# Kernel optimization log

Hardware: AMD Instinct MI355X
Metric: run time of the kernel (lower is better)

The kernel has to match this reference:

```python
import jax, jax.numpy as jnp
import numpy as np
from jax.ops import segment_sum, segment_max

N = 20000   # nodes per node type (glom, imm)
E = 320000  # edges per edge type (avg degree 16)
D = 256     # feature dim (in == out, required by GIN's (1+eps)*x + aggr)
LN_EPS = 1e-5


def _ln_relu(x, gamma, beta):
    mu = jnp.mean(x, axis=-1, keepdims=True)
    var = jnp.mean((x - mu) ** 2, axis=-1, keepdims=True)
    return jax.nn.relu((x - mu) * jax.lax.rsqrt(var + LN_EPS) * gamma + beta)


def _forward(x_glom, x_imm, ew_gg, ea_ig, W_gcn, b_gcn, Wl, bl, Wr, br, att, We,
             b_gat, eps, W_gin, b_gin, gamma, beta, ei_gg, ei_ig, ei_gi):
    # ---- GCNConv on (glom->glom): add_self_loops=True, edge_weight=ew_gg ----
    src, dst = ei_gg[0], ei_gg[1]
    xw = x_glom @ W_gcn                                   # [N, D]
    deg = segment_sum(ew_gg, dst, num_segments=N) + 1.0   # +1 for self-loop weight
    dinv = jax.lax.rsqrt(deg)                             # [N]
    coef = dinv[src] * ew_gg * dinv[dst]                  # [E] symmetric gcn_norm
    out_gcn = segment_sum(coef[:, None] * xw[src], dst, num_segments=N)
    out_gcn = out_gcn + (dinv * dinv)[:, None] * xw + b_gcn  # self-loop + bias

    # ---- GATv2Conv on (imm->glom): heads=1, edge_dim=1, no self loops ----
    s, d = ei_ig[0], ei_ig[1]
    hl = x_imm @ Wl + bl          # lin_l on source  [N, D]
    hr = x_glom @ Wr + br         # lin_r on target  [N, D]
    he = ea_ig @ We               # lin_edge         [E, D]
    z = jax.nn.leaky_relu(hl[s] + hr[d] + he, 0.2)
    logits = z @ att              # [E]
    m = segment_max(logits, d, num_segments=N)            # stable segment softmax
    ex = jnp.exp(logits - m[d])
    denom = segment_sum(ex, d, num_segments=N)
    alpha = ex / denom[d]
    out_gat = segment_sum(alpha[:, None] * hl[s], d, num_segments=N) + b_gat

    # ---- GINConv on (glom->imm): nn = Linear, train_eps ----
    s2, d2 = ei_gi[0], ei_gi[1]
    agg = segment_sum(x_glom[s2], d2, num_segments=N)     # sum aggregation
    out_gin = ((1.0 + eps[0]) * x_imm + agg) @ W_gin + b_gin

    # HeteroConv(aggr='sum') across edge types per destination node type,
    # then shared LayerNorm + ReLU
    glom = _ln_relu(out_gcn + out_gat, gamma, beta)
    imm = _ln_relu(out_gin, gamma, beta)
    return glom, imm


def setup_inputs() -> dict:
    key = jax.random.key(0)
    k = jax.random.split(key, 13)
    s = 0.06  # ~ glorot-ish scale for D=256
    return {
        'x_glom': jax.random.normal(k[0], (N, D), jnp.float32),
        'x_imm': jax.random.normal(k[1], (N, D), jnp.float32),
        'ew_gg': jax.random.uniform(k[2], (E,), jnp.float32),
        'ea_ig': jax.random.normal(k[3], (E, 1), jnp.float32),
        'W_gcn': jax.random.normal(k[4], (D, D), jnp.float32) * s,
        'b_gcn': jnp.zeros((D,), jnp.float32),
        'Wl': jax.random.normal(k[5], (D, D), jnp.float32) * s,
        'bl': jnp.zeros((D,), jnp.float32),
        'Wr': jax.random.normal(k[6], (D, D), jnp.float32) * s,
        'br': jnp.zeros((D,), jnp.float32),
        'att': jax.random.normal(k[7], (D,), jnp.float32) * s,
        'We': jax.random.normal(k[8], (1, D), jnp.float32) * s,
        'b_gat': jnp.zeros((D,), jnp.float32),
        'eps': jnp.zeros((1,), jnp.float32),
        'W_gin': jax.random.normal(k[9], (D, D), jnp.float32) * s,
        'b_gin': jnp.zeros((D,), jnp.float32),
        'gamma': jnp.ones((D,), jnp.float32),
        'beta': jnp.zeros((D,), jnp.float32),
        'ei_gg': jax.random.randint(k[10], (2, E), 0, N),
        'ei_ig': jax.random.randint(k[11], (2, E), 0, N),
        'ei_gi': jax.random.randint(k[12], (2, E), 0, N),
    }


def reference(x_glom, x_imm, ew_gg, ea_ig, W_gcn, b_gcn, Wl, bl, Wr, br, att, We,
              b_gat, eps, W_gin, b_gin, gamma, beta, ei_gg, ei_ig, ei_gi):
    return _forward(x_glom, x_imm, ew_gg, ea_ig, W_gcn, b_gcn, Wl, bl, Wr, br,
                    att, We, b_gat, eps, W_gin, b_gin, gamma, beta,
                    ei_gg, ei_ig, ei_gi)
```

## Files before the change

kernel.cpp:

```cpp
#include <hip/hip_runtime.h>


constexpr int D = 256;

typedef __attribute__((ext_vector_type(4))) float f32x4v;
typedef __attribute__((ext_vector_type(8))) short short8;

__device__ __forceinline__ float4 ld4(const float* p) {
    return *reinterpret_cast<const float4*>(p);
}
__device__ __forceinline__ void st4(float* p, float4 v) {
    *reinterpret_cast<float4*>(p) = v;
}
__device__ __forceinline__ unsigned short f2bf(float f) {
    unsigned u = __float_as_uint(f);
    u = u + 0x7FFFu + ((u >> 16) & 1u);
    return (unsigned short)(u >> 16);
}
__device__ __forceinline__ float bf2f(unsigned short u) {
    return __uint_as_float(((unsigned)u) << 16);
}
__device__ __forceinline__ float4 ldb4(const unsigned short* p) {
    ushort4 u = *reinterpret_cast<const ushort4*>(p);
    return make_float4(bf2f(u.x), bf2f(u.y), bf2f(u.z), bf2f(u.w));
}
__device__ __forceinline__ float wave_sum(float p) {
#pragma unroll
    for (int off = 32; off > 0; off >>= 1) p += __shfl_xor(p, off, 64);
    return p;
}
__device__ __forceinline__ float gat_partial(float4 h, float4 hrv, float ea,
                                             float4 We4, float4 att4) {
    float z, pp = 0.f;
    z = h.x + hrv.x + ea * We4.x; z *= (z > 0.f) ? 1.0f : 0.2f; pp += z * att4.x;
    z = h.y + hrv.y + ea * We4.y; z *= (z > 0.f) ? 1.0f : 0.2f; pp += z * att4.y;
    z = h.z + hrv.z + ea * We4.z; z *= (z > 0.f) ? 1.0f : 0.2f; pp += z * att4.z;
    z = h.w + hrv.w + ea * We4.w; z *= (z > 0.f) ? 1.0f : 0.2f; pp += z * att4.w;
    return pp;
}

__global__ __launch_bounds__(256)
void k_front(const float* __restrict__ x_glom, const float* __restrict__ x_imm,
             unsigned short* __restrict__ xb_glom, unsigned short* __restrict__ xb_imm,
             const float* __restrict__ W0, const float* __restrict__ W1,
             const float* __restrict__ W2, const float* __restrict__ W3,
             unsigned short* __restrict__ Wt,
             const int* __restrict__ ei_gg, const int* __restrict__ ei_ig,
             const int* __restrict__ ei_gi, const float* __restrict__ ew_gg,
             int* __restrict__ counts, int* __restrict__ rank,
             float* __restrict__ degsum,
             int n4, int nbCast, int nbHist, int E, int N)
{
    int bx = blockIdx.x;
    if (bx < 2 * nbCast) {
        bool second = (bx >= nbCast);
        int i = (second ? bx - nbCast : bx) * 256 + threadIdx.x;
        if (i < n4) {
            const float* x = second ? x_imm : x_glom;
            unsigned short* y = second ? xb_imm : xb_glom;
            float4 v = ld4(x + (size_t)i * 4);
            ushort4 o;
            o.x = f2bf(v.x); o.y = f2bf(v.y); o.z = f2bf(v.z); o.w = f2bf(v.w);
            *reinterpret_cast<ushort4*>(y + (size_t)i * 4) = o;
        }
        return;
    }
    bx -= 2 * nbCast;
    if (bx < 1024) {
        int w = bx >> 8;
        int i = ((bx & 255) << 8) + threadIdx.x;
        const float* W = (w == 0) ? W0 : (w == 1) ? W1 : (w == 2) ? W2 : W3;
        int c = i >> 8, k = i & 255;
        Wt[(size_t)w * D * D + i] = f2bf(W[k * D + c]);
        return;
    }
    bx -= 1024;
    {
        int t = bx / nbHist;
        int e = (bx - t * nbHist) * 256 + threadIdx.x;
        if (e >= E) return;
        const int* ei = (t == 0) ? ei_gg : (t == 1) ? ei_ig : ei_gi;
        int d = ei[E + e];
        rank[(size_t)t * E + e] = atomicAdd(&counts[t * N + d], 1);
        if (t == 0) atomicAdd(&degsum[d], ew_gg[e]);
    }
}

__global__ __launch_bounds__(256)
void k_scan_tile(const int* __restrict__ counts, int* __restrict__ rows,
                 int* __restrict__ partials, int N, int TPT)
{
    int t = blockIdx.y, tile = blockIdx.x;
    int i = tile * 256 + threadIdx.x;
    __shared__ int sh[256];
    int v = (i < N) ? counts[(size_t)t * N + i] : 0;
    sh[threadIdx.x] = v;
    __syncthreads();
#pragma unroll
    for (int off = 1; off < 256; off <<= 1) {
        int add = (threadIdx.x >= off) ? sh[threadIdx.x - off] : 0;
        __syncthreads();
        sh[threadIdx.x] += add;
        __syncthreads();
    }
    if (i < N) rows[(size_t)t * (N + 1) + i] = sh[threadIdx.x] - v;
    if (threadIdx.x == 255) partials[t * TPT + tile] = sh[255];
}

__global__ __launch_bounds__(128)
void k_scan_part(int* __restrict__ partials, int TPT)
{
    int t = blockIdx.x;
    __shared__ int sh[128];
    int v = (threadIdx.x < TPT) ? partials[t * TPT + threadIdx.x] : 0;
    sh[threadIdx.x] = v;
    __syncthreads();
#pragma unroll
    for (int off = 1; off < 128; off <<= 1) {
        int add = (threadIdx.x >= off) ? sh[threadIdx.x - off] : 0;
        __syncthreads();
        sh[threadIdx.x] += add;
        __syncthreads();
    }
    if (threadIdx.x < TPT) partials[t * TPT + threadIdx.x] = sh[threadIdx.x] - v;
}

__global__ void k_scan_final(int* __restrict__ rows, const int* __restrict__ partials,
                             int N, int TPT, int E)
{
    int i = blockIdx.x * 256 + threadIdx.x;
    if (i >= 3 * N) return;
    int t = i / N, j = i - t * N;
    rows[(size_t)t * (N + 1) + j] += partials[t * TPT + (j >> 8)];
    if (j == 0) rows[(size_t)t * (N + 1) + N] = E;
}

__global__ __launch_bounds__(256)
void k_mid(
           const unsigned short* __restrict__ xbg,
           const unsigned short* __restrict__ xbi,
           const unsigned short* __restrict__ Wt,
           const float* __restrict__ degsum,
           const float* __restrict__ br, const float* __restrict__ bl,
           unsigned short* __restrict__ xws, unsigned short* __restrict__ hr,
           unsigned short* __restrict__ hl,
           const int* __restrict__ ei_gg, const int* __restrict__ ei_ig,
           const int* __restrict__ ei_gi, const float* __restrict__ ew_gg,
           const float* __restrict__ ea_ig,
           const int* __restrict__ rows, const int* __restrict__ rank,
           int2* __restrict__ pk_gcn, int2* __restrict__ pk_gat,
           int* __restrict__ src_gin,
           int nbProjRow, int nbProj, int nbE, int E, int N, int M)
{
    int bx = blockIdx.x;
    if (bx < nbProj) {
        int brow = bx / 12;
        int yy   = bx - brow * 12;
        const int lane = threadIdx.x & 63;
        const int wave = threadIdx.x >> 6;
        const int lr = lane & 15;
        const int lk = lane >> 4;
        const int row0 = brow * 256 + wave * 64;

        const unsigned short* A;
        const unsigned short* Bt0;
        int col0;
        if (yy < 8) { A = xbg; Bt0 = Wt;             col0 = yy * 64; }
        else        { A = xbi; Bt0 = Wt + 2 * D * D; col0 = (yy - 8) * 64; }

        const unsigned short* ap[4];
#pragma unroll
        for (int rf = 0; rf < 4; ++rf) {
            int arow = row0 + rf * 16 + lr;
            int arow_c = (arow < M) ? arow : (M - 1);
            ap[rf] = A + (size_t)arow_c * D + lk * 8;
        }
        const unsigned short* bp = Bt0 + (size_t)(col0 + lr) * D + lk * 8;

        f32x4v acc[4][4] = {};
#pragma unroll
        for (int k0 = 0; k0 < 256; k0 += 32) {
            short8 af[4], bf[4];
#pragma unroll
            for (int rf = 0; rf < 4; ++rf)
                af[rf] = *reinterpret_cast<const short8*>(ap[rf] + k0);
#pragma unroll
            for (int nf = 0; nf < 4; ++nf)
                bf[nf] = *reinterpret_cast<const short8*>(bp + (size_t)nf * 16 * D + k0);
#pragma unroll
            for (int rf = 0; rf < 4; ++rf)
#pragma unroll
                for (int nf = 0; nf < 4; ++nf)
                    acc[rf][nf] = __builtin_amdgcn_mfma_f32_16x16x32_bf16(
                        af[rf], bf[nf], acc[rf][nf], 0, 0, 0);
        }

#pragma unroll
        for (int nf = 0; nf < 4; ++nf) {
            int c = col0 + nf * 16 + lr;
            unsigned short* dst;
            int cc;
            float bv;
            bool scaled;
            if (yy < 8) {
                if (c < 256) { dst = xws; cc = c;       bv = 0.f;    scaled = true;  }
                else         { dst = hr;  cc = c - 256; bv = br[cc]; scaled = false; }
            } else           { dst = hl;  cc = c;       bv = bl[cc]; scaled = false; }
#pragma unroll
            for (int rf = 0; rf < 4; ++rf) {
#pragma unroll
                for (int i = 0; i < 4; ++i) {
                    int r = row0 + rf * 16 + 4 * lk + i;
                    if (r < M) {
                        float sc = scaled ? rsqrtf(1.0f + degsum[r]) : 1.0f;
                        dst[(size_t)r * D + cc] = f2bf(acc[rf][nf][i] * sc + bv);
                    }
                }
            }
        }
        return;
    }
    int sx = bx - nbProj;
    int t = sx / nbE;
    int e = (sx - t * nbE) * 256 + threadIdx.x;
    if (e >= E) return;
    if (t == 0) {
        int s = ei_gg[e], d = ei_gg[E + e];
        int pos = rows[d] + rank[e];
        pk_gcn[pos] = make_int2(s, __float_as_int(ew_gg[e]));
    } else if (t == 1) {
        int s = ei_ig[e], d = ei_ig[E + e];
        int pos = rows[(N + 1) + d] + rank[(size_t)E + e];
        pk_gat[pos] = make_int2(s, __float_as_int(ea_ig[e]));
    } else {
        int s = ei_gi[e], d = ei_gi[E + e];
        int pos = rows[2 * (N + 1) + d] + rank[2 * (size_t)E + e];
        src_gin[pos] = s;
    }
}

__global__ __launch_bounds__(256)
void k_gin_gemm_ln(const unsigned short* __restrict__ A,
                   const unsigned short* __restrict__ Bt,
                   const float* __restrict__ bias,
                   const float* __restrict__ gamma, const float* __restrict__ beta,
                   float* __restrict__ out, int M)
{
    __shared__ float lds_s[4][64];
    __shared__ float lds_q[4][64];
    const int lane = threadIdx.x & 63;
    const int wave = threadIdx.x >> 6;
    const int lr = lane & 15;
    const int lk = lane >> 4;
    const int row0 = blockIdx.x * 64;
    const int col0 = wave * 64;

    const unsigned short* ap[4];
#pragma unroll
    for (int rf = 0; rf < 4; ++rf) {
        int arow = row0 + rf * 16 + lr;
        int arow_c = (arow < M) ? arow : (M - 1);
        ap[rf] = A + (size_t)arow_c * D + lk * 8;
    }
    const unsigned short* bp = Bt + (size_t)(col0 + lr) * D + lk * 8;

    f32x4v acc[4][4] = {};
#pragma unroll
    for (int k0 = 0; k0 < 256; k0 += 32) {
        short8 af[4], bf[4];
#pragma unroll
        for (int rf = 0; rf < 4; ++rf)
            af[rf] = *reinterpret_cast<const short8*>(ap[rf] + k0);
#pragma unroll
        for (int nf = 0; nf < 4; ++nf)
            bf[nf] = *reinterpret_cast<const short8*>(bp + (size_t)nf * 16 * D + k0);
#pragma unroll
        for (int rf = 0; rf < 4; ++rf)
#pragma unroll
            for (int nf = 0; nf < 4; ++nf)
                acc[rf][nf] = __builtin_amdgcn_mfma_f32_16x16x32_bf16(
                    af[rf], bf[nf], acc[rf][nf], 0, 0, 0);
    }

    float bv[4], gv[4], be[4];
#pragma unroll
    for (int nf = 0; nf < 4; ++nf) {
        int c = col0 + nf * 16 + lr;
        bv[nf] = bias[c]; gv[nf] = gamma[c]; be[nf] = beta[c];
    }

#pragma unroll
    for (int rf = 0; rf < 4; ++rf) {
        float ps[4], pq[4];
#pragma unroll
        for (int i = 0; i < 4; ++i) {
            float s = 0.f, q = 0.f;
#pragma unroll
            for (int nf = 0; nf < 4; ++nf) {
                float v = acc[rf][nf][i] + bv[nf];
                acc[rf][nf][i] = v;
                s += v; q += v * v;
            }
            ps[i] = s; pq[i] = q;
        }
#pragma unroll
        for (int off = 1; off < 16; off <<= 1) {
#pragma unroll
            for (int i = 0; i < 4; ++i) {
                ps[i] += __shfl_xor(ps[i], off, 64);
                pq[i] += __shfl_xor(pq[i], off, 64);
            }
        }
        if (lr == 0) {
#pragma unroll
            for (int i = 0; i < 4; ++i) {
                lds_s[wave][rf * 16 + lk * 4 + i] = ps[i];
                lds_q[wave][rf * 16 + lk * 4 + i] = pq[i];
            }
        }
    }
    __syncthreads();

#pragma unroll
    for (int rf = 0; rf < 4; ++rf) {
#pragma unroll
        for (int i = 0; i < 4; ++i) {
            int rl = rf * 16 + 4 * lk + i;
            float s = lds_s[0][rl] + lds_s[1][rl] + lds_s[2][rl] + lds_s[3][rl];
            float q = lds_q[0][rl] + lds_q[1][rl] + lds_q[2][rl] + lds_q[3][rl];
            float mu  = s * (1.0f / 256.0f);
            float var = q * (1.0f / 256.0f) - mu * mu;
            float rs  = rsqrtf(var + 1e-5f);
            int r = row0 + rl;
            if (r < M) {
#pragma unroll
                for (int nf = 0; nf < 4; ++nf) {
                    out[(size_t)r * D + col0 + nf * 16 + lr] =
                        fmaxf(0.f, (acc[rf][nf][i] - mu) * rs * gv[nf] + be[nf]);
                }
            }
        }
    }
}

__global__ __launch_bounds__(256)
void k_gather_fused(const unsigned short* __restrict__ xws,
                    const unsigned short* __restrict__ hl,
                    const unsigned short* __restrict__ hr,
                    const float* __restrict__ degsum,
                    const int* __restrict__ rows_gcn, const int2* __restrict__ pk_gcn,
                    const int* __restrict__ rows_gat, const int2* __restrict__ pk_gat,
                    const float* __restrict__ We, const float* __restrict__ att,
                    const float* __restrict__ b_gcn, const float* __restrict__ b_gat,
                    const float* __restrict__ gamma, const float* __restrict__ beta,
                    float* __restrict__ glom_out,
                    const unsigned short* __restrict__ xb_glom,
                    const float* __restrict__ x_imm, const float* __restrict__ eps,
                    const int* __restrict__ rows_gin, const int* __restrict__ src_gin,
                    unsigned short* __restrict__ agg,
                    int N)
{
    int gw   = __builtin_amdgcn_readfirstlane((blockIdx.x * 256 + threadIdx.x) >> 6);
    int lane = threadIdx.x & 63;

    if (gw < N) {
        int node = gw;
        float4 We4  = ld4(&We[lane * 4]);
        float4 att4 = ld4(&att[lane * 4]);
        float4 hrv  = ldb4(&hr[(size_t)node * D + lane * 4]);

        float di = rsqrtf(1.0f + degsum[node]);
        float4 acc = ldb4(&xws[(size_t)node * D + lane * 4]);
        float4 g0  = ld4(&b_gcn[lane * 4]);
        float4 a0  = ld4(&b_gat[lane * 4]);
        acc.x = di * acc.x + g0.x + a0.x;
        acc.y = di * acc.y + g0.y + a0.y;
        acc.z = di * acc.z + g0.z + a0.z;
        acc.w = di * acc.w + g0.w + a0.w;

        int p  = rows_gcn[node];
        int p1 = rows_gcn[node + 1];
        int2 pkn[4];
        if (p + 4 <= p1) {
#pragma unroll
            for (int j = 0; j < 4; ++j) pkn[j] = pk_gcn[p + j];
        }
        while (p + 4 <= p1) {
            int2 pkc[4];
#pragma unroll
            for (int j = 0; j < 4; ++j) pkc[j] = pkn[j];
            p += 4;
            if (p + 4 <= p1) {
#pragma unroll
                for (int j = 0; j < 4; ++j) pkn[j] = pk_gcn[p + j];
            }
            float cf[4];
            float4 v[4];
#pragma unroll
            for (int j = 0; j < 4; ++j) cf[j] = __int_as_float(pkc[j].y) * di;
#pragma unroll
            for (int j = 0; j < 4; ++j) v[j] = ldb4(&xws[(size_t)pkc[j].x * D + lane * 4]);
#pragma unroll
            for (int j = 0; j < 4; ++j) {
                acc.x += cf[j] * v[j].x; acc.y += cf[j] * v[j].y;
                acc.z += cf[j] * v[j].z; acc.w += cf[j] * v[j].w;
            }
        }
        for (; p < p1; ++p) {
            int2 pk = pk_gcn[p];
            float cx = __int_as_float(pk.y) * di;
            float4 v = ldb4(&xws[(size_t)pk.x * D + lane * 4]);
            acc.x += cx * v.x; acc.y += cx * v.y;
            acc.z += cx * v.z; acc.w += cx * v.w;
        }

        int q  = rows_gat[node];
        int q1 = rows_gat[node + 1];
        int has = (q1 > q);
        float m = -3.4e38f, den = 0.f;
        float4 ag = make_float4(0.f, 0.f, 0.f, 0.f);
        int2 qkn[4];
        if (q + 4 <= q1) {
#pragma unroll
            for (int j = 0; j < 4; ++j) qkn[j] = pk_gat[q + j];
        }
        while (q + 4 <= q1) {
            int2 qkc[4];
#pragma unroll
            for (int j = 0; j < 4; ++j) qkc[j] = qkn[j];
            q += 4;
            if (q + 4 <= q1) {
#pragma unroll
                for (int j = 0; j < 4; ++j) qkn[j] = pk_gat[q + j];
            }
            float4 h[4];
            float pp[4];
#pragma unroll
            for (int j = 0; j < 4; ++j) h[j] = ldb4(&hl[(size_t)qkc[j].x * D + lane * 4]);
#pragma unroll
            for (int j = 0; j < 4; ++j)
                pp[j] = wave_sum(gat_partial(h[j], hrv, __int_as_float(qkc[j].y), We4, att4));
            float mb = fmaxf(fmaxf(pp[0], pp[1]), fmaxf(pp[2], pp[3]));
            float mn = fmaxf(m, mb);
            float scale = __expf(m - mn);
            float x[4];
#pragma unroll
            for (int j = 0; j < 4; ++j) x[j] = __expf(pp[j] - mn);
            den = den * scale + (x[0] + x[1]) + (x[2] + x[3]);
            float axx = 0.f, ayy = 0.f, azz = 0.f, aww = 0.f;
#pragma unroll
            for (int j = 0; j < 4; ++j) {
                axx += x[j] * h[j].x; ayy += x[j] * h[j].y;
                azz += x[j] * h[j].z; aww += x[j] * h[j].w;
            }
            ag.x = ag.x * scale + axx; ag.y = ag.y * scale + ayy;
            ag.z = ag.z * scale + azz; ag.w = ag.w * scale + aww;
            m = mn;
        }
        for (; q < q1; ++q) {
            int2 pk = pk_gat[q];
            float4 h = ldb4(&hl[(size_t)pk.x * D + lane * 4]);
            float pp = wave_sum(gat_partial(h, hrv, __int_as_float(pk.y), We4, att4));
            float mn = fmaxf(m, pp);
            float scale = __expf(m - mn);
            float ex = __expf(pp - mn);
            den = den * scale + ex;
            ag.x = ag.x * scale + ex * h.x;
            ag.y = ag.y * scale + ex * h.y;
            ag.z = ag.z * scale + ex * h.z;
            ag.w = ag.w * scale + ex * h.w;
            m = mn;
        }
        if (has) {
            float inv = 1.0f / den;
            acc.x += ag.x * inv; acc.y += ag.y * inv;
            acc.z += ag.z * inv; acc.w += ag.w * inv;
        }

        float s_ = acc.x + acc.y + acc.z + acc.w;
        float sq = acc.x * acc.x + acc.y * acc.y + acc.z * acc.z + acc.w * acc.w;
#pragma unroll
        for (int off = 32; off > 0; off >>= 1) {
            s_ += __shfl_xor(s_, off, 64);
            sq += __shfl_xor(sq, off, 64);
        }
        float mu  = s_ * (1.0f / 256.0f);
        float var = sq * (1.0f / 256.0f) - mu * mu;
        float rs  = rsqrtf(var + 1e-5f);
        float4 g = ld4(&gamma[lane * 4]);
        float4 b = ld4(&beta[lane * 4]);
        float4 o;
        o.x = fmaxf(0.f, (acc.x - mu) * rs * g.x + b.x);
        o.y = fmaxf(0.f, (acc.y - mu) * rs * g.y + b.y);
        o.z = fmaxf(0.f, (acc.z - mu) * rs * g.z + b.z);
        o.w = fmaxf(0.f, (acc.w - mu) * rs * g.w + b.w);
        st4(&glom_out[(size_t)node * D + lane * 4], o);
    } else if (gw < 2 * N) {
        int node = gw - N;
        float c = 1.0f + eps[0];
        float4 acc = ld4(&x_imm[(size_t)node * D + lane * 4]);
        acc.x *= c; acc.y *= c; acc.z *= c; acc.w *= c;
        int p  = rows_gin[node];
        int p1 = rows_gin[node + 1];
        int sn[4];
        if (p + 4 <= p1) {
#pragma unroll
            for (int j = 0; j < 4; ++j) sn[j] = src_gin[p + j];
        }
        while (p + 4 <= p1) {
            int sc[4];
#pragma unroll
            for (int j = 0; j < 4; ++j) sc[j] = sn[j];
            p += 4;
            if (p + 4 <= p1) {
#pragma unroll
                for (int j = 0; j < 4; ++j) sn[j] = src_gin[p + j];
            }
            float4 v[4];
#pragma unroll
            for (int j = 0; j < 4; ++j) v[j] = ldb4(&xb_glom[(size_t)sc[j] * D + lane * 4]);
            acc.x += (v[0].x + v[1].x) + (v[2].x + v[3].x);
            acc.y += (v[0].y + v[1].y) + (v[2].y + v[3].y);
            acc.z += (v[0].z + v[1].z) + (v[2].z + v[3].z);
            acc.w += (v[0].w + v[1].w) + (v[2].w + v[3].w);
        }
        for (; p < p1; ++p) {
            int sx = src_gin[p];
            float4 v = ldb4(&xb_glom[(size_t)sx * D + lane * 4]);
            acc.x += v.x; acc.y += v.y; acc.z += v.z; acc.w += v.w;
        }
        ushort4 o;
        o.x = f2bf(acc.x); o.y = f2bf(acc.y); o.z = f2bf(acc.z); o.w = f2bf(acc.w);
        *reinterpret_cast<ushort4*>(agg + (size_t)node * D + lane * 4) = o;
    }
}

extern "C" void kernel_launch(void* const* d_in, const int* in_sizes, int n_in,
                              void* d_out, int out_size, void* d_ws, size_t ws_size,
                              hipStream_t stream)
{
    const float* x_glom = (const float*)d_in[0];
    const float* x_imm  = (const float*)d_in[1];
    const float* ew_gg  = (const float*)d_in[2];
    const float* ea_ig  = (const float*)d_in[3];
    const float* W_gcn  = (const float*)d_in[4];
    const float* b_gcn  = (const float*)d_in[5];
    const float* Wl     = (const float*)d_in[6];
    const float* bl     = (const float*)d_in[7];
    const float* Wr     = (const float*)d_in[8];
    const float* br     = (const float*)d_in[9];
    const float* att    = (const float*)d_in[10];
    const float* We     = (const float*)d_in[11];
    const float* b_gat  = (const float*)d_in[12];
    const float* eps    = (const float*)d_in[13];
    const float* W_gin  = (const float*)d_in[14];
    const float* b_gin  = (const float*)d_in[15];
    const float* gamma  = (const float*)d_in[16];
    const float* beta   = (const float*)d_in[17];
    const int*   ei_gg  = (const int*)d_in[18];
    const int*   ei_ig  = (const int*)d_in[19];
    const int*   ei_gi  = (const int*)d_in[20];

    const int N = in_sizes[0] / D;
    const int E = in_sizes[2];
    const size_t ND = (size_t)N * D;
    const int TPT = (N + 255) / 256;

    char* base = (char*)d_ws;
    size_t off = 0;
    auto alloc = [&](size_t bytes) {
        void* p = base + off;
        off = (off + bytes + 255) & ~(size_t)255;
        return p;
    };
    unsigned short* xb_glom = (unsigned short*)alloc(ND * 2);
    unsigned short* xb_imm  = (unsigned short*)alloc(ND * 2);
    unsigned short* xws_b   = (unsigned short*)alloc(ND * 2);
    unsigned short* hl_b    = (unsigned short*)alloc(ND * 2);
    unsigned short* hr_b    = (unsigned short*)alloc(ND * 2);
    unsigned short* agg_b   = (unsigned short*)alloc(ND * 2);
    unsigned short* Wt      = (unsigned short*)alloc(4 * D * D * 2);
    int*   counts  = (int*)alloc(3 * (size_t)N * 4 + (size_t)N * 4);
    float* degsum  = (float*)(counts + 3 * (size_t)N);
    int*   rows    = (int*)alloc(3 * (size_t)(N + 1) * 4);
    int*   parts   = (int*)alloc(3 * (size_t)TPT * 4);
    int*   rank    = (int*)alloc(3 * (size_t)E * 4);
    int2*  pk_gcn  = (int2*)alloc((size_t)E * 8);
    int2*  pk_gat  = (int2*)alloc((size_t)E * 8);
    int*   src_gin = (int*)alloc((size_t)E * 4);

    float* glom_out = (float*)d_out;
    float* imm_out  = (float*)d_out + ND;

    const int n4      = (int)(ND / 4);
    const int nbCast  = (n4 + 255) / 256;
    const int nbHist  = (E + 255) / 256;
    const int nb_3n   = (3 * N + 255) / 256;
    const int nb_2nw  = (2 * N + 3) / 4;
    const int nbProjRow = (N + 255) / 256;
    const int nbProj    = nbProjRow * 12;

    hipMemsetAsync(counts, 0, 4 * (size_t)N * 4, stream);
    k_front<<<2 * nbCast + 1024 + 3 * nbHist, 256, 0, stream>>>(
        x_glom, x_imm, xb_glom, xb_imm,
        W_gcn, Wr, Wl, W_gin, Wt,
        ei_gg, ei_ig, ei_gi, ew_gg,
        counts, rank, degsum, n4, nbCast, nbHist, E, N);
    k_scan_tile<<<dim3(TPT, 3), 256, 0, stream>>>(counts, rows, parts, N, TPT);
    k_scan_part<<<3, 128, 0, stream>>>(parts, TPT);
    k_scan_final<<<nb_3n, 256, 0, stream>>>(rows, parts, N, TPT, E);
    k_mid<<<nbProj + 3 * nbHist, 256, 0, stream>>>(
        xb_glom, xb_imm, Wt, degsum, br, bl, xws_b, hr_b, hl_b,
        ei_gg, ei_ig, ei_gi, ew_gg, ea_ig,
        rows, rank, pk_gcn, pk_gat, src_gin,
        nbProjRow, nbProj, nbHist, E, N, N);
    k_gather_fused<<<nb_2nw, 256, 0, stream>>>(
        xws_b, hl_b, hr_b, degsum,
        rows, pk_gcn,
        rows + (N + 1), pk_gat,
        We, att, b_gcn, b_gat, gamma, beta, glom_out,
        xb_glom, x_imm, eps,
        rows + 2 * (N + 1), src_gin, agg_b, N);
    k_gin_gemm_ln<<<(N + 63) / 64, 256, 0, stream>>>(
        agg_b, Wt + 3 * D * D, b_gin, gamma, beta, imm_out, N);
}
```

Before: 240.4 us.

## Apply GIN linear before aggregation and fuse GIN into the gather kernel

Uses linearity to compute x_glom@W_gin and x_imm@W_gin inside the projection GEMM, so the GIN branch becomes a gather-sum of pre-projected rows followed by LayerNorm in the gather kernel. This removes the separate GIN GEMM+LN kernel and the agg intermediate buffer. The gather kernel is also restructured so each wave processes two edges at once, each half-wave loading 8 bf16 values (16 bytes) per lane, with cross-half reductions for the GCN sums and for the GAT online softmax. The histogram blocks are moved to the front of k_front. In exchange the projection GEMM grows from 12 to 20 column tiles per row block, and rounding to bf16 now happens before aggregation rather than after.

```diff
diff --git a/kernel.cpp b/kernel.cpp
--- a/kernel.cpp
+++ b/kernel.cpp
@@ -8,9 +8,6 @@
 
 __device__ __forceinline__ float4 ld4(const float* p) {
     return *reinterpret_cast<const float4*>(p);
-}
-__device__ __forceinline__ void st4(float* p, float4 v) {
-    *reinterpret_cast<float4*>(p) = v;
 }
 __device__ __forceinline__ unsigned short f2bf(float f) {
     unsigned u = __float_as_uint(f);
@@ -20,23 +17,10 @@
 __device__ __forceinline__ float bf2f(unsigned short u) {
     return __uint_as_float(((unsigned)u) << 16);
 }
-__device__ __forceinline__ float4 ldb4(const unsigned short* p) {
-    ushort4 u = *reinterpret_cast<const ushort4*>(p);
-    return make_float4(bf2f(u.x), bf2f(u.y), bf2f(u.z), bf2f(u.w));
-}
-__device__ __forceinline__ float wave_sum(float p) {
-#pragma unroll
-    for (int off = 32; off > 0; off >>= 1) p += __shfl_xor(p, off, 64);
-    return p;
-}
-__device__ __forceinline__ float gat_partial(float4 h, float4 hrv, float ea,
-                                             float4 We4, float4 att4) {
-    float z, pp = 0.f;
-    z = h.x + hrv.x + ea * We4.x; z *= (z > 0.f) ? 1.0f : 0.2f; pp += z * att4.x;
-    z = h.y + hrv.y + ea * We4.y; z *= (z > 0.f) ? 1.0f : 0.2f; pp += z * att4.y;
-    z = h.z + hrv.z + ea * We4.z; z *= (z > 0.f) ? 1.0f : 0.2f; pp += z * att4.z;
-    z = h.w + hrv.w + ea * We4.w; z *= (z > 0.f) ? 1.0f : 0.2f; pp += z * att4.w;
-    return pp;
+__device__ __forceinline__ void ldbf8(const unsigned short* p, float* o) {
+    short8 u = *reinterpret_cast<const short8*>(p);
+#pragma unroll
+    for (int j = 0; j < 8; ++j) o[j] = bf2f((unsigned short)u[j]);
 }
 
 __global__ __launch_bounds__(256)
@@ -52,6 +36,17 @@
              int n4, int nbCast, int nbHist, int E, int N)
 {
     int bx = blockIdx.x;
+    if (bx < 3 * nbHist) {
+        int t = bx / nbHist;
+        int e = (bx - t * nbHist) * 256 + threadIdx.x;
+        if (e >= E) return;
+        const int* ei = (t == 0) ? ei_gg : (t == 1) ? ei_ig : ei_gi;
+        int d = ei[E + e];
+        rank[(size_t)t * E + e] = atomicAdd(&counts[t * N + d], 1);
+        if (t == 0) atomicAdd(&degsum[d], ew_gg[e]);
+        return;
+    }
+    bx -= 3 * nbHist;
     if (bx < 2 * nbCast) {
         bool second = (bx >= nbCast);
         int i = (second ? bx - nbCast : bx) * 256 + threadIdx.x;
@@ -66,23 +61,12 @@
         return;
     }
     bx -= 2 * nbCast;
-    if (bx < 1024) {
+    {
         int w = bx >> 8;
         int i = ((bx & 255) << 8) + threadIdx.x;
         const float* W = (w == 0) ? W0 : (w == 1) ? W1 : (w == 2) ? W2 : W3;
         int c = i >> 8, k = i & 255;
         Wt[(size_t)w * D * D + i] = f2bf(W[k * D + c]);
-        return;
-    }
-    bx -= 1024;
-    {
-        int t = bx / nbHist;
-        int e = (bx - t * nbHist) * 256 + threadIdx.x;
-        if (e >= E) return;
-        const int* ei = (t == 0) ? ei_gg : (t == 1) ? ei_ig : ei_gi;
-        int d = ei[E + e];
-        rank[(size_t)t * E + e] = atomicAdd(&counts[t * N + d], 1);
-        if (t == 0) atomicAdd(&degsum[d], ew_gg[e]);
     }
 }
 
@@ -136,26 +120,26 @@
 }
 
 __global__ __launch_bounds__(256)
-void k_mid(
-           const unsigned short* __restrict__ xbg,
+void k_mid(const unsigned short* __restrict__ xbg,
            const unsigned short* __restrict__ xbi,
            const unsigned short* __restrict__ Wt,
            const float* __restrict__ degsum,
            const float* __restrict__ br, const float* __restrict__ bl,
            unsigned short* __restrict__ xws, unsigned short* __restrict__ hr,
            unsigned short* __restrict__ hl,
+           unsigned short* __restrict__ xgw, unsigned short* __restrict__ xiw,
            const int* __restrict__ ei_gg, const int* __restrict__ ei_ig,
            const int* __restrict__ ei_gi, const float* __restrict__ ew_gg,
            const float* __restrict__ ea_ig,
            const int* __restrict__ rows, const int* __restrict__ rank,
            int2* __restrict__ pk_gcn, int2* __restrict__ pk_gat,
            int* __restrict__ src_gin,
-           int nbProjRow, int nbProj, int nbE, int E, int N, int M)
+           int nbProj, int nbE, int E, int N, int M)
 {
     int bx = blockIdx.x;
     if (bx < nbProj) {
-        int brow = bx / 12;
-        int yy   = bx - brow * 12;
+        int brow = bx / 20;
+        int yy   = bx - brow * 20;
         const int lane = threadIdx.x & 63;
         const int wave = threadIdx.x >> 6;
         const int lr = lane & 15;
@@ -165,8 +149,10 @@
         const unsigned short* A;
         const unsigned short* Bt0;
         int col0;
-        if (yy < 8) { A = xbg; Bt0 = Wt;             col0 = yy * 64; }
-        else        { A = xbi; Bt0 = Wt + 2 * D * D; col0 = (yy - 8) * 64; }
+        if (yy < 8)       { A = xbg; Bt0 = Wt;             col0 = yy * 64; }
+        else if (yy < 12) { A = xbg; Bt0 = Wt + 3 * D * D; col0 = (yy - 8) * 64; }
+        else if (yy < 16) { A = xbi; Bt0 = Wt + 2 * D * D; col0 = (yy - 12) * 64; }
+        else              { A = xbi; Bt0 = Wt + 3 * D * D; col0 = (yy - 16) * 64; }
 
         const unsigned short* ap[4];
 #pragma unroll
@@ -205,7 +191,9 @@
             if (yy < 8) {
                 if (c < 256) { dst = xws; cc = c;       bv = 0.f;    scaled = true;  }
                 else         { dst = hr;  cc = c - 256; bv = br[cc]; scaled = false; }
-            } else           { dst = hl;  cc = c;       bv = bl[cc]; scaled = false; }
+            } else if (yy < 12) { dst = xgw; cc = c;    bv = 0.f;    scaled = false; }
+            else if (yy < 16)   { dst = hl;  cc = c;    bv = bl[cc]; scaled = false; }
+            else                { dst = xiw; cc = c;    bv = 0.f;    scaled = false; }
 #pragma unroll
             for (int rf = 0; rf < 4; ++rf) {
 #pragma unroll
@@ -240,298 +228,225 @@
 }
 
 __global__ __launch_bounds__(256)
-void k_gin_gemm_ln(const unsigned short* __restrict__ A,
-                   const unsigned short* __restrict__ Bt,
-                   const float* __restrict__ bias,
-                   const float* __restrict__ gamma, const float* __restrict__ beta,
-                   float* __restrict__ out, int M)
-{
-    __shared__ float lds_s[4][64];
-    __shared__ float lds_q[4][64];
-    const int lane = threadIdx.x & 63;
-    const int wave = threadIdx.x >> 6;
-    const int lr = lane & 15;
-    const int lk = lane >> 4;
-    const int row0 = blockIdx.x * 64;
-    const int col0 = wave * 64;
-
-    const unsigned short* ap[4];
-#pragma unroll
-    for (int rf = 0; rf < 4; ++rf) {
-        int arow = row0 + rf * 16 + lr;
-        int arow_c = (arow < M) ? arow : (M - 1);
-        ap[rf] = A + (size_t)arow_c * D + lk * 8;
-    }
-    const unsigned short* bp = Bt + (size_t)(col0 + lr) * D + lk * 8;
-
-    f32x4v acc[4][4] = {};
-#pragma unroll
-    for (int k0 = 0; k0 < 256; k0 += 32) {
-        short8 af[4], bf[4];
-#pragma unroll
-        for (int rf = 0; rf < 4; ++rf)
-            af[rf] = *reinterpret_cast<const short8*>(ap[rf] + k0);
-#pragma unroll
-        for (int nf = 0; nf < 4; ++nf)
-            bf[nf] = *reinterpret_cast<const short8*>(bp + (size_t)nf * 16 * D + k0);
-#pragma unroll
-        for (int rf = 0; rf < 4; ++rf)
-#pragma unroll
-            for (int nf = 0; nf < 4; ++nf)
-                acc[rf][nf] = __builtin_amdgcn_mfma_f32_16x16x32_bf16(
-                    af[rf], bf[nf], acc[rf][nf], 0, 0, 0);
-    }
-
-    float bv[4], gv[4], be[4];
-#pragma unroll
-    for (int nf = 0; nf < 4; ++nf) {
-        int c = col0 + nf * 16 + lr;
-        bv[nf] = bias[c]; gv[nf] = gamma[c]; be[nf] = beta[c];
-    }
-
-#pragma unroll
-    for (int rf = 0; rf < 4; ++rf) {
-        float ps[4], pq[4];
-#pragma unroll
-        for (int i = 0; i < 4; ++i) {
-            float s = 0.f, q = 0.f;
-#pragma unroll
-            for (int nf = 0; nf < 4; ++nf) {
-                float v = acc[rf][nf][i] + bv[nf];
-                acc[rf][nf][i] = v;
-                s += v; q += v * v;
-            }
-            ps[i] = s; pq[i] = q;
-        }
-#pragma unroll
-        for (int off = 1; off < 16; off <<= 1) {
-#pragma unroll
-            for (int i = 0; i < 4; ++i) {
-                ps[i] += __shfl_xor(ps[i], off, 64);
-                pq[i] += __shfl_xor(pq[i], off, 64);
-            }
-        }
-        if (lr == 0) {
-#pragma unroll
-            for (int i = 0; i < 4; ++i) {
-                lds_s[wave][rf * 16 + lk * 4 + i] = ps[i];
-                lds_q[wave][rf * 16 + lk * 4 + i] = pq[i];
-            }
-        }
-    }
-    __syncthreads();
-
-#pragma unroll
-    for (int rf = 0; rf < 4; ++rf) {
-#pragma unroll
-        for (int i = 0; i < 4; ++i) {
-            int rl = rf * 16 + 4 * lk + i;
-            float s = lds_s[0][rl] + lds_s[1][rl] + lds_s[2][rl] + lds_s[3][rl];
-            float q = lds_q[0][rl] + lds_q[1][rl] + lds_q[2][rl] + lds_q[3][rl];
-            float mu  = s * (1.0f / 256.0f);
-            float var = q * (1.0f / 256.0f) - mu * mu;
-            float rs  = rsqrtf(var + 1e-5f);
-            int r = row0 + rl;
-            if (r < M) {
-#pragma unroll
-                for (int nf = 0; nf < 4; ++nf) {
-                    out[(size_t)r * D + col0 + nf * 16 + lr] =
-                        fmaxf(0.f, (acc[rf][nf][i] - mu) * rs * gv[nf] + be[nf]);
-                }
-            }
-        }
-    }
-}
-
-__global__ __launch_bounds__(256)
-void k_gather_fused(const unsigned short* __restrict__ xws,
-                    const unsigned short* __restrict__ hl,
-                    const unsigned short* __restrict__ hr,
-                    const float* __restrict__ degsum,
-                    const int* __restrict__ rows_gcn, const int2* __restrict__ pk_gcn,
-                    const int* __restrict__ rows_gat, const int2* __restrict__ pk_gat,
-                    const float* __restrict__ We, const float* __restrict__ att,
-                    const float* __restrict__ b_gcn, const float* __restrict__ b_gat,
-                    const float* __restrict__ gamma, const float* __restrict__ beta,
-                    float* __restrict__ glom_out,
-                    const unsigned short* __restrict__ xb_glom,
-                    const float* __restrict__ x_imm, const float* __restrict__ eps,
-                    const int* __restrict__ rows_gin, const int* __restrict__ src_gin,
-                    unsigned short* __restrict__ agg,
-                    int N)
+void k_gather2(const unsigned short* __restrict__ xws,
+               const unsigned short* __restrict__ hl,
+               const unsigned short* __restrict__ hr,
+               const float* __restrict__ degsum,
+               const int* __restrict__ rows_gcn, const int2* __restrict__ pk_gcn,
+               const int* __restrict__ rows_gat, const int2* __restrict__ pk_gat,
+               const float* __restrict__ We, const float* __restrict__ att,
+               const float* __restrict__ b_gcn, const float* __restrict__ b_gat,
+               const float* __restrict__ gamma, const float* __restrict__ beta,
+               float* __restrict__ glom_out,
+               const unsigned short* __restrict__ xgw,
+               const unsigned short* __restrict__ xiw,
+               const float* __restrict__ eps, const float* __restrict__ b_gin,
+               const int* __restrict__ rows_gin, const int* __restrict__ src_gin,
+               float* __restrict__ imm_out,
+               int N)
 {
     int gw   = __builtin_amdgcn_readfirstlane((blockIdx.x * 256 + threadIdx.x) >> 6);
     int lane = threadIdx.x & 63;
+    int sl   = lane & 31;
+    int half = lane >> 5;
+    int c0   = sl * 8;
 
     if (gw < N) {
         int node = gw;
-        float4 We4  = ld4(&We[lane * 4]);
-        float4 att4 = ld4(&att[lane * 4]);
-        float4 hrv  = ldb4(&hr[(size_t)node * D + lane * 4]);
-
         float di = rsqrtf(1.0f + degsum[node]);
-        float4 acc = ldb4(&xws[(size_t)node * D + lane * 4]);
-        float4 g0  = ld4(&b_gcn[lane * 4]);
-        float4 a0  = ld4(&b_gat[lane * 4]);
-        acc.x = di * acc.x + g0.x + a0.x;
-        acc.y = di * acc.y + g0.y + a0.y;
-        acc.z = di * acc.z + g0.z + a0.z;
-        acc.w = di * acc.w + g0.w + a0.w;
-
+
+        float accN[8] = {};
         int p  = rows_gcn[node];
         int p1 = rows_gcn[node + 1];
-        int2 pkn[4];
-        if (p + 4 <= p1) {
-#pragma unroll
-            for (int j = 0; j < 4; ++j) pkn[j] = pk_gcn[p + j];
-        }
-        while (p + 4 <= p1) {
-            int2 pkc[4];
-#pragma unroll
-            for (int j = 0; j < 4; ++j) pkc[j] = pkn[j];
-            p += 4;
-            if (p + 4 <= p1) {
-#pragma unroll
-                for (int j = 0; j < 4; ++j) pkn[j] = pk_gcn[p + j];
-            }
-            float cf[4];
-            float4 v[4];
-#pragma unroll
-            for (int j = 0; j < 4; ++j) cf[j] = __int_as_float(pkc[j].y) * di;
-#pragma unroll
-            for (int j = 0; j < 4; ++j) v[j] = ldb4(&xws[(size_t)pkc[j].x * D + lane * 4]);
-#pragma unroll
-            for (int j = 0; j < 4; ++j) {
-                acc.x += cf[j] * v[j].x; acc.y += cf[j] * v[j].y;
-                acc.z += cf[j] * v[j].z; acc.w += cf[j] * v[j].w;
-            }
-        }
-        for (; p < p1; ++p) {
-            int2 pk = pk_gcn[p];
-            float cx = __int_as_float(pk.y) * di;
-            float4 v = ldb4(&xws[(size_t)pk.x * D + lane * 4]);
-            acc.x += cx * v.x; acc.y += cx * v.y;
-            acc.z += cx * v.z; acc.w += cx * v.w;
-        }
+        for (; p + 4 <= p1; p += 4) {
+            int2 e0 = pk_gcn[p + 0], e1 = pk_gcn[p + 1];
+            int2 e2 = pk_gcn[p + 2], e3 = pk_gcn[p + 3];
+            int sA = half ? e1.x : e0.x;
+            int sB = half ? e3.x : e2.x;
+            float wA = __int_as_float(half ? e1.y : e0.y) * di;
+            float wB = __int_as_float(half ? e3.y : e2.y) * di;
+            float rA[8], rB[8];
+            ldbf8(&xws[(size_t)sA * D + c0], rA);
+            ldbf8(&xws[(size_t)sB * D + c0], rB);
+#pragma unroll
+            for (int j = 0; j < 8; ++j) accN[j] += wA * rA[j] + wB * rB[j];
+        }
+        for (; p < p1; p += 2) {
+            int i1 = (p + 1 < p1) ? p + 1 : p;
+            float vf = (p + 1 < p1 || half == 0) ? 1.0f : 0.0f;
+            int2 e0 = pk_gcn[p], e1 = pk_gcn[i1];
+            int s = half ? e1.x : e0.x;
+            float w = __int_as_float(half ? e1.y : e0.y) * di * vf;
+            float r[8];
+            ldbf8(&xws[(size_t)s * D + c0], r);
+#pragma unroll
+            for (int j = 0; j < 8; ++j) accN[j] += w * r[j];
+        }
+
+        float We8[8], att8[8], hrv[8];
+        ldbf8(&hr[(size_t)node * D + c0], hrv);
+#pragma unroll
+        for (int j = 0; j < 8; ++j) { We8[j] = We[c0 + j]; att8[j] = att[c0 + j]; }
 
         int q  = rows_gat[node];
         int q1 = rows_gat[node + 1];
         int has = (q1 > q);
         float m = -3.4e38f, den = 0.f;
-        float4 ag = make_float4(0.f, 0.f, 0.f, 0.f);
-        int2 qkn[4];
-        if (q + 4 <= q1) {
-#pragma unroll
-            for (int j = 0; j < 4; ++j) qkn[j] = pk_gat[q + j];
-        }
-        while (q + 4 <= q1) {
-            int2 qkc[4];
-#pragma unroll
-            for (int j = 0; j < 4; ++j) qkc[j] = qkn[j];
-            q += 4;
-            if (q + 4 <= q1) {
-#pragma unroll
-                for (int j = 0; j < 4; ++j) qkn[j] = pk_gat[q + j];
+        float ag[8] = {};
+
+        auto gat_pp = [&](const float* h, float ea) -> float {
+            float pp = 0.f;
+#pragma unroll
+            for (int j = 0; j < 8; ++j) {
+                float z = h[j] + hrv[j] + ea * We8[j];
+                z *= (z > 0.f) ? 1.0f : 0.2f;
+                pp += z * att8[j];
             }
-            float4 h[4];
-            float pp[4];
-#pragma unroll
-            for (int j = 0; j < 4; ++j) h[j] = ldb4(&hl[(size_t)qkc[j].x * D + lane * 4]);
-#pragma unroll
-            for (int j = 0; j < 4; ++j)
-                pp[j] = wave_sum(gat_partial(h[j], hrv, __int_as_float(qkc[j].y), We4, att4));
-            float mb = fmaxf(fmaxf(pp[0], pp[1]), fmaxf(pp[2], pp[3]));
-            float mn = fmaxf(m, mb);
+#pragma unroll
+            for (int off = 16; off > 0; off >>= 1) pp += __shfl_xor(pp, off, 64);
+            return pp;
+        };
+
+        for (; q + 4 <= q1; q += 4) {
+            int2 e0 = pk_gat[q + 0], e1 = pk_gat[q + 1];
+            int2 e2 = pk_gat[q + 2], e3 = pk_gat[q + 3];
+            int sA = half ? e1.x : e0.x;
+            int sB = half ? e3.x : e2.x;
+            float eaA = __int_as_float(half ? e1.y : e0.y);
+            float eaB = __int_as_float(half ? e3.y : e2.y);
+            float hA[8], hB[8];
+            ldbf8(&hl[(size_t)sA * D + c0], hA);
+            ldbf8(&hl[(size_t)sB * D + c0], hB);
+            float ppA = gat_pp(hA, eaA);
+            float ppB = gat_pp(hB, eaB);
+            float mn = fmaxf(m, fmaxf(ppA, ppB));
             float scale = __expf(m - mn);
-            float x[4];
-#pragma unroll
-            for (int j = 0; j < 4; ++j) x[j] = __expf(pp[j] - mn);
-            den = den * scale + (x[0] + x[1]) + (x[2] + x[3]);
-            float axx = 0.f, ayy = 0.f, azz = 0.f, aww = 0.f;
-#pragma unroll
-            for (int j = 0; j < 4; ++j) {
-                axx += x[j] * h[j].x; ayy += x[j] * h[j].y;
-                azz += x[j] * h[j].z; aww += x[j] * h[j].w;
-            }
-            ag.x = ag.x * scale + axx; ag.y = ag.y * scale + ayy;
-            ag.z = ag.z * scale + azz; ag.w = ag.w * scale + aww;
+            float xA = __expf(ppA - mn);
+            float xB = __expf(ppB - mn);
+            den = den * scale + xA + xB;
+#pragma unroll
+            for (int j = 0; j < 8; ++j)
+                ag[j] = ag[j] * scale + xA * hA[j] + xB * hB[j];
             m = mn;
         }
-        for (; q < q1; ++q) {
-            int2 pk = pk_gat[q];
-            float4 h = ldb4(&hl[(size_t)pk.x * D + lane * 4]);
-            float pp = wave_sum(gat_partial(h, hrv, __int_as_float(pk.y), We4, att4));
+        for (; q < q1; q += 2) {
+            int i1 = (q + 1 < q1) ? q + 1 : q;
+            float vf = (q + 1 < q1 || half == 0) ? 1.0f : 0.0f;
+            int2 e0 = pk_gat[q], e1 = pk_gat[i1];
+            int s = half ? e1.x : e0.x;
+            float ea = __int_as_float(half ? e1.y : e0.y);
+            float h[8];
+            ldbf8(&hl[(size_t)s * D + c0], h);
+            float pp = gat_pp(h, ea);
             float mn = fmaxf(m, pp);
             float scale = __expf(m - mn);
-            float ex = __expf(pp - mn);
-            den = den * scale + ex;
-            ag.x = ag.x * scale + ex * h.x;
-            ag.y = ag.y * scale + ex * h.y;
-            ag.z = ag.z * scale + ex * h.z;
-            ag.w = ag.w * scale + ex * h.w;
+            float x = __expf(pp - mn) * vf;
+            den = den * scale + x;
+#pragma unroll
+            for (int j = 0; j < 8; ++j) ag[j] = ag[j] * scale + x * h[j];
             m = mn;
         }
+
+#pragma unroll
+        for (int j = 0; j < 8; ++j) accN[j] += __shfl_xor(accN[j], 32, 64);
+
+        float acc[8];
+        {
+            float xw8[8];
+            ldbf8(&xws[(size_t)node * D + c0], xw8);
+#pragma unroll
+            for (int j = 0; j < 8; ++j)
+                acc[j] = di * xw8[j] + b_gcn[c0 + j] + b_gat[c0 + j] + accN[j];
+        }
         if (has) {
-            float inv = 1.0f / den;
-            acc.x += ag.x * inv; acc.y += ag.y * inv;
-            acc.z += ag.z * inv; acc.w += ag.w * inv;
-        }
-
-        float s_ = acc.x + acc.y + acc.z + acc.w;
-        float sq = acc.x * acc.x + acc.y * acc.y + acc.z * acc.z + acc.w * acc.w;
-#pragma unroll
-        for (int off = 32; off > 0; off >>= 1) {
+            float mo  = __shfl_xor(m, 32, 64);
+            float dno = __shfl_xor(den, 32, 64);
+            float mt  = fmaxf(m, mo);
+            float se  = __expf(m - mt);
+            float so  = __expf(mo - mt);
+            float dent = den * se + dno * so;
+            float inv = 1.0f / dent;
+#pragma unroll
+            for (int j = 0; j < 8; ++j) {
+                float agt = ag[j] * se + __shfl_xor(ag[j], 32, 64) * so;
+                acc[j] += agt * inv;
+            }
+        }
+
+        float s_ = 0.f, sq = 0.f;
+#pragma unroll
+        for (int j = 0; j < 8; ++j) { s_ += acc[j]; sq += acc[j] * acc[j]; }
+#pragma unroll
+        for (int off = 16; off > 0; off >>= 1) {
             s_ += __shfl_xor(s_, off, 64);
             sq += __shfl_xor(sq, off, 64);
         }
         float mu  = s_ * (1.0f / 256.0f);
         float var = sq * (1.0f / 256.0f) - mu * mu;
         float rs  = rsqrtf(var + 1e-5f);
-        float4 g = ld4(&gamma[lane * 4]);
-        float4 b = ld4(&beta[lane * 4]);
         float4 o;
-        o.x = fmaxf(0.f, (acc.x - mu) * rs * g.x + b.x);
-        o.y = fmaxf(0.f, (acc.y - mu) * rs * g.y + b.y);
-        o.z = fmaxf(0.f, (acc.z - mu) * rs * g.z + b.z);
-        o.w = fmaxf(0.f, (acc.w - mu) * rs * g.w + b.w);
-        st4(&glom_out[(size_t)node * D + lane * 4], o);
+        int cb = c0 + half * 4;
+#pragma unroll
+        for (int jj = 0; jj < 4; ++jj) {
+            float v = (acc[half * 4 + jj] - mu) * rs * gamma[cb + jj] + beta[cb + jj];
+            (&o.x)[jj] = fmaxf(0.f, v);
+        }
+        *reinterpret_cast<float4*>(&glom_out[(size_t)node * D + cb]) = o;
     } else if (gw < 2 * N) {
         int node = gw - N;
-        float c = 1.0f + eps[0];
-        float4 acc = ld4(&x_imm[(size_t)node * D + lane * 4]);
-        acc.x *= c; acc.y *= c; acc.z *= c; acc.w *= c;
+        float accN[8] = {};
         int p  = rows_gin[node];
         int p1 = rows_gin[node + 1];
-        int sn[4];
-        if (p + 4 <= p1) {
-#pragma unroll
-            for (int j = 0; j < 4; ++j) sn[j] = src_gin[p + j];
-        }
-        while (p + 4 <= p1) {
-            int sc[4];
-#pragma unroll
-            for (int j = 0; j < 4; ++j) sc[j] = sn[j];
-            p += 4;
-            if (p + 4 <= p1) {
-#pragma unroll
-                for (int j = 0; j < 4; ++j) sn[j] = src_gin[p + j];
-            }
-            float4 v[4];
-#pragma unroll
-            for (int j = 0; j < 4; ++j) v[j] = ldb4(&xb_glom[(size_t)sc[j] * D + lane * 4]);
-            acc.x += (v[0].x + v[1].x) + (v[2].x + v[3].x);
-            acc.y += (v[0].y + v[1].y) + (v[2].y + v[3].y);
-            acc.z += (v[0].z + v[1].z) + (v[2].z + v[3].z);
-            acc.w += (v[0].w + v[1].w) + (v[2].w + v[3].w);
-        }
-        for (; p < p1; ++p) {
-            int sx = src_gin[p];
-            float4 v = ldb4(&xb_glom[(size_t)sx * D + lane * 4]);
-            acc.x += v.x; acc.y += v.y; acc.z += v.z; acc.w += v.w;
-        }
-        ushort4 o;
-        o.x = f2bf(acc.x); o.y = f2bf(acc.y); o.z = f2bf(acc.z); o.w = f2bf(acc.w);
-        *reinterpret_cast<ushort4*>(agg + (size_t)node * D + lane * 4) = o;
+        for (; p + 4 <= p1; p += 4) {
+            int sA = src_gin[p + half];
+            int sB = src_gin[p + 2 + half];
+            float rA[8], rB[8];
+            ldbf8(&xgw[(size_t)sA * D + c0], rA);
+            ldbf8(&xgw[(size_t)sB * D + c0], rB);
+#pragma unroll
+            for (int j = 0; j < 8; ++j) accN[j] += rA[j] + rB[j];
+        }
+        for (; p < p1; p += 2) {
+            int i1 = (p + 1 < p1) ? p + 1 : p;
+            float vf = (p + 1 < p1 || half == 0) ? 1.0f : 0.0f;
+            int s = half ? src_gin[i1] : src_gin[p];
+            float r[8];
+            ldbf8(&xgw[(size_t)s * D + c0], r);
+#pragma unroll
+            for (int j = 0; j < 8; ++j) accN[j] += vf * r[j];
+        }
+#pragma unroll
+        for (int j = 0; j < 8; ++j) accN[j] += __shfl_xor(accN[j], 32, 64);
+
+        float ce = 1.0f + eps[0];
+        float acc[8];
+        {
+            float xi8[8];
+            ldbf8(&xiw[(size_t)node * D + c0], xi8);
+#pragma unroll
+            for (int j = 0; j < 8; ++j)
+                acc[j] = ce * xi8[j] + b_gin[c0 + j] + accN[j];
+        }
+
+        float s_ = 0.f, sq = 0.f;
+#pragma unroll
+        for (int j = 0; j < 8; ++j) { s_ += acc[j]; sq += acc[j] * acc[j]; }
+#pragma unroll
+        for (int off = 16; off > 0; off >>= 1) {
+            s_ += __shfl_xor(s_, off, 64);
+            sq += __shfl_xor(sq, off, 64);
+        }
+        float mu  = s_ * (1.0f / 256.0f);
+        float var = sq * (1.0f / 256.0f) - mu * mu;
+        float rs  = rsqrtf(var + 1e-5f);
+        float4 o;
+        int cb = c0 + half * 4;
+#pragma unroll
+        for (int jj = 0; jj < 4; ++jj) {
+            float v = (acc[half * 4 + jj] - mu) * rs * gamma[cb + jj] + beta[cb + jj];
+            (&o.x)[jj] = fmaxf(0.f, v);
+        }
+        *reinterpret_cast<float4*>(&imm_out[(size_t)node * D + cb]) = o;
     }
 }
 
@@ -578,7 +493,8 @@
     unsigned short* xws_b   = (unsigned short*)alloc(ND * 2);
     unsigned short* hl_b    = (unsigned short*)alloc(ND * 2);
     unsigned short* hr_b    = (unsigned short*)alloc(ND * 2);
-    unsigned short* agg_b   = (unsigned short*)alloc(ND * 2);
+    unsigned short* xgw_b   = (unsigned short*)alloc(ND * 2);
+    unsigned short* xiw_b   = (unsigned short*)alloc(ND * 2);
     unsigned short* Wt      = (unsigned short*)alloc(4 * D * D * 2);
     int*   counts  = (int*)alloc(3 * (size_t)N * 4 + (size_t)N * 4);
     float* degsum  = (float*)(counts + 3 * (size_t)N);
@@ -598,10 +514,10 @@
     const int nb_3n   = (3 * N + 255) / 256;
     const int nb_2nw  = (2 * N + 3) / 4;
     const int nbProjRow = (N + 255) / 256;
-    const int nbProj    = nbProjRow * 12;
+    const int nbProj    = nbProjRow * 20;
 
     hipMemsetAsync(counts, 0, 4 * (size_t)N * 4, stream);
-    k_front<<<2 * nbCast + 1024 + 3 * nbHist, 256, 0, stream>>>(
+    k_front<<<3 * nbHist + 2 * nbCast + 1024, 256, 0, stream>>>(
         x_glom, x_imm, xb_glom, xb_imm,
         W_gcn, Wr, Wl, W_gin, Wt,
         ei_gg, ei_ig, ei_gi, ew_gg,
@@ -610,17 +526,16 @@
     k_scan_part<<<3, 128, 0, stream>>>(parts, TPT);
     k_scan_final<<<nb_3n, 256, 0, stream>>>(rows, parts, N, TPT, E);
     k_mid<<<nbProj + 3 * nbHist, 256, 0, stream>>>(
-        xb_glom, xb_imm, Wt, degsum, br, bl, xws_b, hr_b, hl_b,
+        xb_glom, xb_imm, Wt, degsum, br, bl,
+        xws_b, hr_b, hl_b, xgw_b, xiw_b,
         ei_gg, ei_ig, ei_gi, ew_gg, ea_ig,
         rows, rank, pk_gcn, pk_gat, src_gin,
-        nbProjRow, nbProj, nbHist, E, N, N);
-    k_gather_fused<<<nb_2nw, 256, 0, stream>>>(
+        nbProj, nbHist, E, N, N);
+    k_gather2<<<nb_2nw, 256, 0, stream>>>(
         xws_b, hl_b, hr_b, degsum,
         rows, pk_gcn,
         rows + (N + 1), pk_gat,
         We, att, b_gcn, b_gat, gamma, beta, glom_out,
-        xb_glom, x_imm, eps,
-        rows + 2 * (N + 1), src_gin, agg_b, N);
-    k_gin_gemm_ln<<<(N + 63) / 64, 256, 0, stream>>>(
-        agg_b, Wt + 3 * D * D, b_gin, gamma, beta, imm_out, N);
-}
+        xgw_b, xiw_b, eps, b_gin,
+        rows + 2 * (N + 1), src_gin, imm_out, N);
+}
```

New measurement: 267.2 us. 1.11x slower.
